# Optimization experiments

Measured on AMD Instinct MI355X. Metric: run time of the kernel, lower is better.

Reference implementation:

```python
import jax, jax.numpy as jnp
import numpy as np

B, N, E, C = 8, 4096, 1024, 512


def setup_inputs() -> dict:
    key = jax.random.key(0)
    k1, k2, k3, k4 = jax.random.split(key, 4)
    node_feats = jax.random.normal(k1, (B, N, C), dtype=jnp.float32)
    hyper_feats = jax.random.normal(k2, (B, E, C), dtype=jnp.float32)
    # torch nn.Linear params: weight [out, in], bias [out]
    Wq = jax.random.normal(k3, (C, C), dtype=jnp.float32) * (1.0 / np.sqrt(C))
    bq = jnp.zeros((C,), dtype=jnp.float32)
    Wkv = jax.random.normal(k4, (2 * C, C), dtype=jnp.float32) * (1.0 / np.sqrt(C))
    bkv = jnp.zeros((2 * C,), dtype=jnp.float32)
    return {"node_feats": node_feats, "hyper_feats": hyper_feats,
            "Wq": Wq, "bq": bq, "Wkv": Wkv, "bkv": bkv}


def reference(node_feats, hyper_feats, Wq, bq, Wkv, bkv):
    C_ = node_feats.shape[-1]
    scale = C_ ** -0.5
    Q = node_feats @ Wq.T + bq                      # [B,N,C]
    KV = hyper_feats @ Wkv.T + bkv                  # [B,E,2C]
    K, V = KV[..., :C_], KV[..., C_:]               # [B,E,C] each
    attn = jnp.einsum('bnc,bec->bne', Q, K) * scale  # [B,N,E]
    attn = jax.nn.softmax(attn, axis=-1)
    return jnp.einsum('bne,bec->bnc', attn, V)       # [B,N,C]
```

## Files before the change

### kernel.cpp

```cpp
#include <hip/hip_runtime.h>
#include <cstdint>
#include <cstddef>

typedef _Float16 h16;
typedef _Float16 h16x4 __attribute__((ext_vector_type(4)));
typedef _Float16 h16x8 __attribute__((ext_vector_type(8)));
typedef float fx4 __attribute__((ext_vector_type(4)));

static constexpr int B_ = 8, N_ = 4096, E_ = 1024, C_ = 512;
static constexpr float SCALE = 0.044194173824159216f;

__device__ __forceinline__ void glds16(const h16* g, h16* l) {
  __builtin_amdgcn_global_load_lds(
      (const __attribute__((address_space(1))) unsigned int*)g,
      (__attribute__((address_space(3))) unsigned int*)l, 16, 0, 0);
}

__global__ __launch_bounds__(256) void cvt_kernel(const float* __restrict__ src,
                                                  h16* __restrict__ dst, int n8) {
  int i = blockIdx.x * 256 + threadIdx.x;
  if (i >= n8) return;
  const float4* s4 = (const float4*)src;
  float4 a = s4[2 * i], b = s4[2 * i + 1];
  h16x8 o;
  o[0] = (h16)a.x; o[1] = (h16)a.y; o[2] = (h16)a.z; o[3] = (h16)a.w;
  o[4] = (h16)b.x; o[5] = (h16)b.y; o[6] = (h16)b.z; o[7] = (h16)b.w;
  *(h16x8*)(dst + (size_t)i * 8) = o;
}

template <int MODE>
__global__ __launch_bounds__(256) void gemm_bt(
    const void* __restrict__ Ap, const h16* __restrict__ Bm,
    const float* __restrict__ bias,
    h16* __restrict__ outH, h16* __restrict__ outK, h16* __restrict__ outVt,
    float* __restrict__ outF,
    int Ncols, int K) {
  constexpr bool CVT = (MODE <= 1);
  __shared__ h16 sA[128 * 32];
  __shared__ h16 sB[128 * 32];
  const int tid = threadIdx.x;
  const int wave = tid >> 6, lane = tid & 63;
  const int wm = wave >> 1, wn = wave & 1;
  const int lr = lane & 15, kq = lane >> 4;
  const int mBase = blockIdx.x * 128, nBase = blockIdx.y * 128;
  const int z = blockIdx.z;
  const h16* Ah = (const h16*)Ap;
  const float* Af = (const float*)Ap;
  if (MODE == 2) { Ah += (size_t)z * N_ * C_; Bm += (size_t)z * E_ * C_; outH += (size_t)z * N_ * E_; }
  if (MODE == 3) { Ah += (size_t)z * N_ * E_; Bm += (size_t)z * C_ * E_; outF += (size_t)z * N_ * C_; }

  fx4 acc[4][4];
#pragma unroll
  for (int i = 0; i < 4; i++)
#pragma unroll
    for (int j = 0; j < 4; j++) acc[i][j] = (fx4){0.f, 0.f, 0.f, 0.f};

  const int rowInA = lane >> 2, colInA = (lane & 3) * 8;
  const int cvtRow = tid >> 1, cvtCol = (tid & 1) * 16;

  for (int kb = 0; kb < K; kb += 32) {
    __syncthreads();
    if (CVT) {
      const float4* src = (const float4*)(Af + (size_t)(mBase + cvtRow) * K + kb + cvtCol);
      float4 f0 = src[0], f1 = src[1], f2 = src[2], f3 = src[3];
      h16x8 p0, p1;
      p0[0] = (h16)f0.x; p0[1] = (h16)f0.y; p0[2] = (h16)f0.z; p0[3] = (h16)f0.w;
      p0[4] = (h16)f1.x; p0[5] = (h16)f1.y; p0[6] = (h16)f1.z; p0[7] = (h16)f1.w;
      p1[0] = (h16)f2.x; p1[1] = (h16)f2.y; p1[2] = (h16)f2.z; p1[3] = (h16)f2.w;
      p1[4] = (h16)f3.x; p1[5] = (h16)f3.y; p1[6] = (h16)f3.z; p1[7] = (h16)f3.w;
      *(h16x8*)&sA[cvtRow * 32 + cvtCol] = p0;
      *(h16x8*)&sA[cvtRow * 32 + cvtCol + 8] = p1;
    } else {
#pragma unroll
      for (int i = 0; i < 2; i++) {
        int chunk = wave + i * 4;
        glds16(Ah + (size_t)(mBase + chunk * 16 + rowInA) * K + kb + colInA,
               &sA[chunk * 512]);
      }
    }
#pragma unroll
    for (int i = 0; i < 2; i++) {
      int chunk = wave + i * 4;
      glds16(Bm + (size_t)(nBase + chunk * 16 + rowInA) * K + kb + colInA,
             &sB[chunk * 512]);
    }
    __syncthreads();
    h16x8 af[4], bf[4];
#pragma unroll
    for (int mi = 0; mi < 4; mi++)
      af[mi] = *(const h16x8*)&sA[(wm * 64 + mi * 16 + lr) * 32 + kq * 8];
#pragma unroll
    for (int ni = 0; ni < 4; ni++)
      bf[ni] = *(const h16x8*)&sB[(wn * 64 + ni * 16 + lr) * 32 + kq * 8];
#pragma unroll
    for (int mi = 0; mi < 4; mi++)
#pragma unroll
      for (int ni = 0; ni < 4; ni++)
        acc[mi][ni] = __builtin_amdgcn_mfma_f32_16x16x32_f16(af[mi], bf[ni], acc[mi][ni], 0, 0, 0);
  }

  const int rb = kq * 4;
#pragma unroll
  for (int mi = 0; mi < 4; mi++) {
#pragma unroll
    for (int ni = 0; ni < 4; ni++) {
      int row0 = mBase + wm * 64 + mi * 16 + rb;
      int col = nBase + wn * 64 + ni * 16 + lr;
      if (MODE == 1 && col >= C_) {
        float bv = bias[col];
        h16x4 pk;
#pragma unroll
        for (int r = 0; r < 4; r++) pk[r] = (h16)(acc[mi][ni][r] + bv);
        int zb = row0 >> 10, e = row0 & 1023;
        *(h16x4*)&outVt[((size_t)zb * C_ + (col - C_)) * E_ + e] = pk;
      } else {
#pragma unroll
        for (int r = 0; r < 4; r++) {
          int row = row0 + r;
          float v = acc[mi][ni][r];
          if (MODE == 0) {
            outH[(size_t)row * Ncols + col] = (h16)(v + bias[col]);
          } else if (MODE == 1) {
            outK[(size_t)row * C_ + col] = (h16)(v + bias[col]);
          } else if (MODE == 2) {
            outH[(size_t)row * Ncols + col] = (h16)(v * SCALE);
          } else {
            outF[(size_t)row * Ncols + col] = v;
          }
        }
      }
    }
  }
}

__global__ __launch_bounds__(256) void softmax_rows(h16* __restrict__ S) {
  int row = blockIdx.x * 4 + (threadIdx.x >> 6);
  int lane = threadIdx.x & 63;
  h16* p = S + (size_t)row * E_ + lane * 16;
  h16x8 q0 = *(const h16x8*)p;
  h16x8 q1 = *(const h16x8*)(p + 8);
  float v[16];
#pragma unroll
  for (int j = 0; j < 8; j++) { v[j] = (float)q0[j]; v[8 + j] = (float)q1[j]; }
  float m = v[0];
#pragma unroll
  for (int j = 1; j < 16; j++) m = fmaxf(m, v[j]);
#pragma unroll
  for (int off = 32; off > 0; off >>= 1) m = fmaxf(m, __shfl_xor(m, off));
  float s = 0.f;
#pragma unroll
  for (int j = 0; j < 16; j++) { v[j] = __expf(v[j] - m); s += v[j]; }
#pragma unroll
  for (int off = 32; off > 0; off >>= 1) s += __shfl_xor(s, off);
  float inv = 1.f / s;
  h16x8 o0, o1;
#pragma unroll
  for (int j = 0; j < 8; j++) { o0[j] = (h16)(v[j] * inv); o1[j] = (h16)(v[8 + j] * inv); }
  *(h16x8*)p = o0;
  *(h16x8*)(p + 8) = o1;
}

extern "C" void kernel_launch(void* const* d_in, const int* in_sizes, int n_in,
                              void* d_out, int out_size, void* d_ws, size_t ws_size,
                              hipStream_t stream) {
  const float* node  = (const float*)d_in[0];
  const float* hyper = (const float*)d_in[1];
  const float* Wq    = (const float*)d_in[2];
  const float* bq    = (const float*)d_in[3];
  const float* Wkv   = (const float*)d_in[4];
  const float* bkv   = (const float*)d_in[5];
  float* out = (float*)d_out;
  char* ws = (char*)d_ws;

  h16* S_h    = (h16*)(ws + 0);
  h16* Q_h    = (h16*)(ws + 67108864);
  h16* K_h    = (h16*)(ws + 100663296);
  h16* Vt_h   = (h16*)(ws + 109051904);
  h16* Wq_h   = (h16*)(ws + 117440512);
  h16* Wkv_h  = (h16*)(ws + 117964800);
  if (ws_size < 119013376u) return;

  cvt_kernel<<<dim3((C_ * C_ / 8 + 255) / 256), 256, 0, stream>>>(Wq, Wq_h, C_ * C_ / 8);
  cvt_kernel<<<dim3((2 * C_ * C_ / 8 + 255) / 256), 256, 0, stream>>>(Wkv, Wkv_h, 2 * C_ * C_ / 8);

  gemm_bt<0><<<dim3(B_ * N_ / 128, C_ / 128), 256, 0, stream>>>(
      node, Wq_h, bq, Q_h, nullptr, nullptr, nullptr, C_, C_);
  gemm_bt<1><<<dim3(B_ * E_ / 128, 2 * C_ / 128), 256, 0, stream>>>(
      hyper, Wkv_h, bkv, nullptr, K_h, Vt_h, nullptr, 2 * C_, C_);
  gemm_bt<2><<<dim3(N_ / 128, E_ / 128, B_), 256, 0, stream>>>(
      Q_h, K_h, nullptr, S_h, nullptr, nullptr, nullptr, E_, C_);
  softmax_rows<<<dim3(B_ * N_ / 4), 256, 0, stream>>>(S_h);
  gemm_bt<3><<<dim3(N_ / 128, C_ / 128, B_), 256, 0, stream>>>(
      S_h, Vt_h, nullptr, nullptr, nullptr, nullptr, out, C_, E_);
}
```

Baseline: 314.2 us.

## Fuse softmax into score GEMM epilogue and normalize in PV GEMM

Removes the separate softmax kernel. The QK^T GEMM epilogue now writes exp(score*scale) directly, without max subtraction, and atomically accumulates per-row sums into a zeroed workspace buffer. The PV GEMM divides by the row sum in its epilogue. The fp32 A-tile conversion loop is also reorganised into narrower, more coalesced float4 loads. Skipping the max subtraction risks fp16 overflow for large logits, and the atomics add contention.

```diff
diff --git a/kernel.cpp b/kernel.cpp
--- a/kernel.cpp
+++ b/kernel.cpp
@@ -33,7 +33,7 @@
     const void* __restrict__ Ap, const h16* __restrict__ Bm,
     const float* __restrict__ bias,
     h16* __restrict__ outH, h16* __restrict__ outK, h16* __restrict__ outVt,
-    float* __restrict__ outF,
+    float* __restrict__ outF, float* __restrict__ rowsum,
     int Ncols, int K) {
   constexpr bool CVT = (MODE <= 1);
   __shared__ h16 sA[128 * 32];
@@ -46,8 +46,10 @@
   const int z = blockIdx.z;
   const h16* Ah = (const h16*)Ap;
   const float* Af = (const float*)Ap;
-  if (MODE == 2) { Ah += (size_t)z * N_ * C_; Bm += (size_t)z * E_ * C_; outH += (size_t)z * N_ * E_; }
-  if (MODE == 3) { Ah += (size_t)z * N_ * E_; Bm += (size_t)z * C_ * E_; outF += (size_t)z * N_ * C_; }
+  if (MODE == 2) { Ah += (size_t)z * N_ * C_; Bm += (size_t)z * E_ * C_;
+                   outH += (size_t)z * N_ * E_; rowsum += (size_t)z * N_; }
+  if (MODE == 3) { Ah += (size_t)z * N_ * E_; Bm += (size_t)z * C_ * E_;
+                   outF += (size_t)z * N_ * C_; rowsum += (size_t)z * N_; }
 
   fx4 acc[4][4];
 #pragma unroll
@@ -56,20 +58,20 @@
     for (int j = 0; j < 4; j++) acc[i][j] = (fx4){0.f, 0.f, 0.f, 0.f};
 
   const int rowInA = lane >> 2, colInA = (lane & 3) * 8;
-  const int cvtRow = tid >> 1, cvtCol = (tid & 1) * 16;
+  const int cvtRow = tid >> 3;
+  const int cvtCol = (tid & 7) * 4;
 
   for (int kb = 0; kb < K; kb += 32) {
     __syncthreads();
     if (CVT) {
-      const float4* src = (const float4*)(Af + (size_t)(mBase + cvtRow) * K + kb + cvtCol);
-      float4 f0 = src[0], f1 = src[1], f2 = src[2], f3 = src[3];
-      h16x8 p0, p1;
-      p0[0] = (h16)f0.x; p0[1] = (h16)f0.y; p0[2] = (h16)f0.z; p0[3] = (h16)f0.w;
-      p0[4] = (h16)f1.x; p0[5] = (h16)f1.y; p0[6] = (h16)f1.z; p0[7] = (h16)f1.w;
-      p1[0] = (h16)f2.x; p1[1] = (h16)f2.y; p1[2] = (h16)f2.z; p1[3] = (h16)f2.w;
-      p1[4] = (h16)f3.x; p1[5] = (h16)f3.y; p1[6] = (h16)f3.z; p1[7] = (h16)f3.w;
-      *(h16x8*)&sA[cvtRow * 32 + cvtCol] = p0;
-      *(h16x8*)&sA[cvtRow * 32 + cvtCol + 8] = p1;
+#pragma unroll
+      for (int j = 0; j < 4; j++) {
+        int row = j * 32 + cvtRow;
+        float4 f = *(const float4*)(Af + (size_t)(mBase + row) * K + kb + cvtCol);
+        h16x4 p;
+        p[0] = (h16)f.x; p[1] = (h16)f.y; p[2] = (h16)f.z; p[3] = (h16)f.w;
+        *(h16x4*)&sA[row * 32 + cvtCol] = p;
+      }
     } else {
 #pragma unroll
       for (int i = 0; i < 2; i++) {
@@ -100,64 +102,65 @@
   }
 
   const int rb = kq * 4;
+  if (MODE == 2) {
 #pragma unroll
-  for (int mi = 0; mi < 4; mi++) {
+    for (int mi = 0; mi < 4; mi++) {
 #pragma unroll
-    for (int ni = 0; ni < 4; ni++) {
-      int row0 = mBase + wm * 64 + mi * 16 + rb;
-      int col = nBase + wn * 64 + ni * 16 + lr;
-      if (MODE == 1 && col >= C_) {
-        float bv = bias[col];
-        h16x4 pk;
+      for (int r = 0; r < 4; r++) {
+        int row = mBase + wm * 64 + mi * 16 + rb + r;
+        float rs = 0.f;
 #pragma unroll
-        for (int r = 0; r < 4; r++) pk[r] = (h16)(acc[mi][ni][r] + bv);
-        int zb = row0 >> 10, e = row0 & 1023;
-        *(h16x4*)&outVt[((size_t)zb * C_ + (col - C_)) * E_ + e] = pk;
-      } else {
+        for (int ni = 0; ni < 4; ni++) {
+          int col = nBase + wn * 64 + ni * 16 + lr;
+          float e = __expf(acc[mi][ni][r] * SCALE);
+          rs += e;
+          outH[(size_t)row * Ncols + col] = (h16)e;
+        }
+        rs += __shfl_xor(rs, 1); rs += __shfl_xor(rs, 2);
+        rs += __shfl_xor(rs, 4); rs += __shfl_xor(rs, 8);
+        if (lr == 0) atomicAdd(&rowsum[row], rs);
+      }
+    }
+  } else if (MODE == 3) {
 #pragma unroll
-        for (int r = 0; r < 4; r++) {
-          int row = row0 + r;
-          float v = acc[mi][ni][r];
-          if (MODE == 0) {
-            outH[(size_t)row * Ncols + col] = (h16)(v + bias[col]);
-          } else if (MODE == 1) {
-            outK[(size_t)row * C_ + col] = (h16)(v + bias[col]);
-          } else if (MODE == 2) {
-            outH[(size_t)row * Ncols + col] = (h16)(v * SCALE);
-          } else {
-            outF[(size_t)row * Ncols + col] = v;
+    for (int mi = 0; mi < 4; mi++) {
+#pragma unroll
+      for (int r = 0; r < 4; r++) {
+        int row = mBase + wm * 64 + mi * 16 + rb + r;
+        float inv = 1.0f / rowsum[row];
+#pragma unroll
+        for (int ni = 0; ni < 4; ni++) {
+          int col = nBase + wn * 64 + ni * 16 + lr;
+          outF[(size_t)row * Ncols + col] = acc[mi][ni][r] * inv;
+        }
+      }
+    }
+  } else {
+#pragma unroll
+    for (int mi = 0; mi < 4; mi++) {
+#pragma unroll
+      for (int ni = 0; ni < 4; ni++) {
+        int row0 = mBase + wm * 64 + mi * 16 + rb;
+        int col = nBase + wn * 64 + ni * 16 + lr;
+        if (MODE == 1 && col >= C_) {
+          float bv = bias[col];
+          h16x4 pk;
+#pragma unroll
+          for (int r = 0; r < 4; r++) pk[r] = (h16)(acc[mi][ni][r] + bv);
+          int zb = row0 >> 10, e = row0 & 1023;
+          *(h16x4*)&outVt[((size_t)zb * C_ + (col - C_)) * E_ + e] = pk;
+        } else {
+#pragma unroll
+          for (int r = 0; r < 4; r++) {
+            int row = row0 + r;
+            float v = acc[mi][ni][r] + bias[col];
+            if (MODE == 0) outH[(size_t)row * Ncols + col] = (h16)v;
+            else           outK[(size_t)row * C_ + col] = (h16)v;
           }
         }
       }
     }
   }
-}
-
-__global__ __launch_bounds__(256) void softmax_rows(h16* __restrict__ S) {
-  int row = blockIdx.x * 4 + (threadIdx.x >> 6);
-  int lane = threadIdx.x & 63;
-  h16* p = S + (size_t)row * E_ + lane * 16;
-  h16x8 q0 = *(const h16x8*)p;
-  h16x8 q1 = *(const h16x8*)(p + 8);
-  float v[16];
-#pragma unroll
-  for (int j = 0; j < 8; j++) { v[j] = (float)q0[j]; v[8 + j] = (float)q1[j]; }
-  float m = v[0];
-#pragma unroll
-  for (int j = 1; j < 16; j++) m = fmaxf(m, v[j]);
-#pragma unroll
-  for (int off = 32; off > 0; off >>= 1) m = fmaxf(m, __shfl_xor(m, off));
-  float s = 0.f;
-#pragma unroll
-  for (int j = 0; j < 16; j++) { v[j] = __expf(v[j] - m); s += v[j]; }
-#pragma unroll
-  for (int off = 32; off > 0; off >>= 1) s += __shfl_xor(s, off);
-  float inv = 1.f / s;
-  h16x8 o0, o1;
-#pragma unroll
-  for (int j = 0; j < 8; j++) { o0[j] = (h16)(v[j] * inv); o1[j] = (h16)(v[8 + j] * inv); }
-  *(h16x8*)p = o0;
-  *(h16x8*)(p + 8) = o1;
 }
 
 extern "C" void kernel_launch(void* const* d_in, const int* in_sizes, int n_in,
@@ -172,24 +175,25 @@
   float* out = (float*)d_out;
   char* ws = (char*)d_ws;
 
-  h16* S_h    = (h16*)(ws + 0);
-  h16* Q_h    = (h16*)(ws + 67108864);
-  h16* K_h    = (h16*)(ws + 100663296);
-  h16* Vt_h   = (h16*)(ws + 109051904);
-  h16* Wq_h   = (h16*)(ws + 117440512);
-  h16* Wkv_h  = (h16*)(ws + 117964800);
-  if (ws_size < 119013376u) return;
+  h16* S_h     = (h16*)(ws + 0);
+  h16* Q_h     = (h16*)(ws + 67108864);
+  h16* K_h     = (h16*)(ws + 100663296);
+  h16* Vt_h    = (h16*)(ws + 109051904);
+  h16* Wq_h    = (h16*)(ws + 117440512);
+  h16* Wkv_h   = (h16*)(ws + 117964800);
+  float* rowsum = (float*)(ws + 119013376);
+  if (ws_size < 119144448u) return;
 
   cvt_kernel<<<dim3((C_ * C_ / 8 + 255) / 256), 256, 0, stream>>>(Wq, Wq_h, C_ * C_ / 8);
   cvt_kernel<<<dim3((2 * C_ * C_ / 8 + 255) / 256), 256, 0, stream>>>(Wkv, Wkv_h, 2 * C_ * C_ / 8);
+  hipMemsetAsync(rowsum, 0, (size_t)B_ * N_ * sizeof(float), stream);
 
   gemm_bt<0><<<dim3(B_ * N_ / 128, C_ / 128), 256, 0, stream>>>(
-      node, Wq_h, bq, Q_h, nullptr, nullptr, nullptr, C_, C_);
+      node, Wq_h, bq, Q_h, nullptr, nullptr, nullptr, nullptr, C_, C_);
   gemm_bt<1><<<dim3(B_ * E_ / 128, 2 * C_ / 128), 256, 0, stream>>>(
-      hyper, Wkv_h, bkv, nullptr, K_h, Vt_h, nullptr, 2 * C_, C_);
+      hyper, Wkv_h, bkv, nullptr, K_h, Vt_h, nullptr, nullptr, 2 * C_, C_);
   gemm_bt<2><<<dim3(N_ / 128, E_ / 128, B_), 256, 0, stream>>>(
-      Q_h, K_h, nullptr, S_h, nullptr, nullptr, nullptr, E_, C_);
-  softmax_rows<<<dim3(B_ * N_ / 4), 256, 0, stream>>>(S_h);
+      Q_h, K_h, nullptr, S_h, nullptr, nullptr, nullptr, rowsum, E_, C_);
   gemm_bt<3><<<dim3(N_ / 128, C_ / 128, B_), 256, 0, stream>>>(
-      S_h, Vt_h, nullptr, nullptr, nullptr, nullptr, out, C_, E_);
+      S_h, Vt_h, nullptr, nullptr, nullptr, nullptr, out, rowsum, C_, E_);
 }
```

Result: no change. 314.1 us (-0.0%).
